# Kernel tuning notes

Hardware: AMD Instinct MI355X
Metric: run time of the kernel (lower is better)

The kernel has to match this reference:

```python
import jax, jax.numpy as jnp
import numpy as np

SCALE = 4          # cfg['stride']
S = 7              # rcnn_crop_size
MAX_SIDE = 64      # max proposal side length in voxels (matches setup_inputs)
# max feature-space crop length = MAX_SIDE/SCALE + 2 (floor/ceil expansion) = 18
WMAX = int(np.ceil((MAX_SIDE // SCALE + 2) / S)) + 1  # = 4, adaptive-pool window bound


def setup_inputs() -> dict:
    key = jax.random.key(0)
    k1, k2, k3, k4 = jax.random.split(key, 4)
    B, C = 2, 128
    D, H, W = 128, 256, 256
    f = jax.random.normal(k1, (B, C, D // SCALE, H // SCALE, W // SCALE), jnp.float32)
    inputs = jnp.zeros((B, 1, D, H, W), jnp.float32)  # only shape is used by forward
    N = 32
    b = jax.random.randint(k2, (N,), 0, B).astype(jnp.float32)
    score = jnp.ones((N,), jnp.float32)
    cz = jax.random.uniform(k3, (N,), minval=32.0, maxval=float(D - 32))
    cy = jax.random.uniform(jax.random.fold_in(k3, 1), (N,), minval=32.0, maxval=float(H - 32))
    cx = jax.random.uniform(jax.random.fold_in(k3, 2), (N,), minval=32.0, maxval=float(W - 32))
    sides = jax.random.randint(k4, (N, 3), 16, MAX_SIDE + 1).astype(jnp.float32)
    proposals = jnp.stack([b, score, cz, cy, cx, sides[:, 0], sides[:, 1], sides[:, 2]], axis=1)
    return {"f": f, "inputs": inputs, "proposals": proposals}


def _crop_pool(f, b, c0, L, feat_dims):
    """Adaptive max-pool3d of f[b, :, c0:c0+L] to [C,S,S,S] via fixed-size masked windows."""
    i = jnp.arange(S)
    # torch adaptive pooling: start=floor(i*L/S), end=ceil((i+1)*L/S)
    start = (i[:, None] * L[None, :]) // S                       # [S,3]
    end = ((i[:, None] + 1) * L[None, :] + S - 1) // S           # [S,3]
    idx = c0[None, :, None] + start[:, :, None] + jnp.arange(WMAX)[None, None, :]  # [S,3,WMAX]
    valid = idx < (c0[None, :, None] + end[:, :, None])
    idx = jnp.minimum(idx, jnp.asarray(feat_dims, jnp.int32)[None, :, None] - 1)
    iz, iy, ix = idx[:, 0], idx[:, 1], idx[:, 2]                 # each [S,WMAX]
    vz, vy, vx = valid[:, 0], valid[:, 1], valid[:, 2]
    # gather [C, S, WMAX, S, WMAX, S, WMAX]
    g = f[b][:, iz[:, :, None, None, None, None],
             iy[None, None, :, :, None, None],
             ix[None, None, None, None, :, :]]
    m = (vz[:, :, None, None, None, None]
         & vy[None, None, :, :, None, None]
         & vx[None, None, None, None, :, :])
    g = jnp.where(m[None], g, -jnp.inf)
    return g.max(axis=(2, 4, 6))  # [C, S, S, S]


def reference(f, inputs, proposals):
    D, H, W = inputs.shape[2:]
    feat_dims = (D // SCALE, H // SCALE, W // SCALE)
    b = proposals[:, 0].astype(jnp.int32)
    center = proposals[:, 2:5]
    side = proposals[:, 5:8]
    c0 = jnp.floor((center - side / 2) / SCALE).astype(jnp.int32)
    c1 = jnp.ceil((center + side / 2) / SCALE).astype(jnp.int32)
    lim = jnp.asarray(feat_dims, jnp.int32)
    c0 = jnp.maximum(c0, 0)
    c1 = jnp.minimum(c1, lim[None, :])
    L = c1 - c0  # [N,3] crop lengths per axis
    pooled = jax.vmap(lambda bb, cc, ll: _crop_pool(f, bb, cc, ll, feat_dims))(b, c0, L)
    return pooled  # [N, C, S, S, S]
```

## Files before the change

kernel.cpp:

```cpp
#include <hip/hip_runtime.h>
#include <math.h>


#define POOL_S 7
constexpr int C_CH = 128;
constexpr int FD = 32, FH = 64, FW = 64;
constexpr int OUT_PER_N = C_CH * POOL_S * POOL_S * POOL_S;
constexpr int TOTAL = 32 * OUT_PER_N;

__global__ __launch_bounds__(256) void crop_roi_kernel(
    const float* __restrict__ f,
    const float* __restrict__ proposals,
    float* __restrict__ out)
{
    int tid = blockIdx.x * blockDim.x + threadIdx.x;
    if (tid >= TOTAL) return;

    int ix = tid % 7;
    int iy = (tid / 7) % 7;
    int iz = (tid / 49) % 7;
    int c  = (tid / 343) % C_CH;
    int n  = tid / OUT_PER_N;

    const float* p = proposals + n * 8;
    int   b  = (int)p[0];
    float cz = p[2], cy = p[3], cx = p[4];
    float sz = p[5], sy = p[6], sx = p[7];

    int c0z = max((int)floorf((cz - sz * 0.5f) * 0.25f), 0);
    int c0y = max((int)floorf((cy - sy * 0.5f) * 0.25f), 0);
    int c0x = max((int)floorf((cx - sx * 0.5f) * 0.25f), 0);
    int c1z = min((int)ceilf((cz + sz * 0.5f) * 0.25f), FD);
    int c1y = min((int)ceilf((cy + sy * 0.5f) * 0.25f), FH);
    int c1x = min((int)ceilf((cx + sx * 0.5f) * 0.25f), FW);
    int Lz = c1z - c0z, Ly = c1y - c0y, Lx = c1x - c0x;

    int z0 = c0z + (iz * Lz) / 7, z1 = c0z + ((iz + 1) * Lz + 6) / 7;
    int y0 = c0y + (iy * Ly) / 7, y1 = c0y + ((iy + 1) * Ly + 6) / 7;
    int x0 = c0x + (ix * Lx) / 7, x1 = c0x + ((ix + 1) * Lx + 6) / 7;

    const float* fb = f + (size_t)(b * C_CH + c) * (FD * FH * FW);

    float m = -INFINITY;
    for (int z = z0; z < z1; ++z) {
        const float* fz = fb + z * (FH * FW);
        for (int y = y0; y < y1; ++y) {
            const float* fy = fz + y * FW;
            for (int x = x0; x < x1; ++x) {
                m = fmaxf(m, fy[x]);
            }
        }
    }
    out[tid] = m;
}

extern "C" void kernel_launch(void* const* d_in, const int* in_sizes, int n_in,
                              void* d_out, int out_size, void* d_ws, size_t ws_size,
                              hipStream_t stream) {
    const float* f         = (const float*)d_in[0];
    const float* proposals = (const float*)d_in[2];
    float* out             = (float*)d_out;

    const int block = 256;
    const int grid  = (TOTAL + block - 1) / block;
    crop_roi_kernel<<<grid, block, 0, stream>>>(f, proposals, out);
}
```

Before: 220.2 us.

## Stage each proposal's crop in LDS and pool windows from shared memory

Each block now handles one proposal and two channels. It first cooperatively loads a padded 17^3 crop of each channel into shared memory, clamping indices to the crop bounds, then computes the 7x7x7 adaptive max-pool windows from LDS. The x loop is replaced by four fixed loads with clamped indices, which relies on each window being at most 4 wide. This removes the redundant, poorly coalesced global reads caused by overlapping pooling windows. In exchange it always loads the full padded 17^3 volume even for small crops and adds a block-wide barrier.

```diff
diff --git a/kernel.cpp b/kernel.cpp
--- a/kernel.cpp
+++ b/kernel.cpp
@@ -2,56 +2,77 @@
 #include <math.h>
 
 
-#define POOL_S 7
 constexpr int C_CH = 128;
 constexpr int FD = 32, FH = 64, FW = 64;
-constexpr int OUT_PER_N = C_CH * POOL_S * POOL_S * POOL_S;
-constexpr int TOTAL = 32 * OUT_PER_N;
+constexpr int CH_VOL = FD * FH * FW;
+constexpr int LMAX = 17;
+constexpr int VOL = LMAX * LMAX * LMAX;
+constexpr int CPB = 2;
+constexpr int THREADS = 256;
 
-__global__ __launch_bounds__(256) void crop_roi_kernel(
+__global__ __launch_bounds__(THREADS) void crop_roi_kernel(
     const float* __restrict__ f,
     const float* __restrict__ proposals,
     float* __restrict__ out)
 {
-    int tid = blockIdx.x * blockDim.x + threadIdx.x;
-    if (tid >= TOTAL) return;
+    __shared__ float lds[CPB * VOL];
 
-    int ix = tid % 7;
-    int iy = (tid / 7) % 7;
-    int iz = (tid / 49) % 7;
-    int c  = (tid / 343) % C_CH;
-    int n  = tid / OUT_PER_N;
+    const int n    = blockIdx.x;
+    const int c0ch = blockIdx.y * CPB;
 
     const float* p = proposals + n * 8;
-    int   b  = (int)p[0];
-    float cz = p[2], cy = p[3], cx = p[4];
-    float sz = p[5], sy = p[6], sx = p[7];
+    const int   b  = (int)p[0];
+    const float cz = p[2], cy = p[3], cx = p[4];
+    const float sz = p[5], sy = p[6], sx = p[7];
 
-    int c0z = max((int)floorf((cz - sz * 0.5f) * 0.25f), 0);
-    int c0y = max((int)floorf((cy - sy * 0.5f) * 0.25f), 0);
-    int c0x = max((int)floorf((cx - sx * 0.5f) * 0.25f), 0);
-    int c1z = min((int)ceilf((cz + sz * 0.5f) * 0.25f), FD);
-    int c1y = min((int)ceilf((cy + sy * 0.5f) * 0.25f), FH);
-    int c1x = min((int)ceilf((cx + sx * 0.5f) * 0.25f), FW);
-    int Lz = c1z - c0z, Ly = c1y - c0y, Lx = c1x - c0x;
+    const int c0z = max((int)floorf((cz - sz * 0.5f) * 0.25f), 0);
+    const int c0y = max((int)floorf((cy - sy * 0.5f) * 0.25f), 0);
+    const int c0x = max((int)floorf((cx - sx * 0.5f) * 0.25f), 0);
+    const int c1z = min((int)ceilf((cz + sz * 0.5f) * 0.25f), FD);
+    const int c1y = min((int)ceilf((cy + sy * 0.5f) * 0.25f), FH);
+    const int c1x = min((int)ceilf((cx + sx * 0.5f) * 0.25f), FW);
+    const int Lz = c1z - c0z, Ly = c1y - c0y, Lx = c1x - c0x;
 
-    int z0 = c0z + (iz * Lz) / 7, z1 = c0z + ((iz + 1) * Lz + 6) / 7;
-    int y0 = c0y + (iy * Ly) / 7, y1 = c0y + ((iy + 1) * Ly + 6) / 7;
-    int x0 = c0x + (ix * Lx) / 7, x1 = c0x + ((ix + 1) * Lx + 6) / 7;
+    const float* fb = f + (size_t)(b * C_CH + c0ch) * CH_VOL
+                        + c0z * (FH * FW) + c0y * FW + c0x;
+    #pragma unroll 4
+    for (int e = threadIdx.x; e < CPB * VOL; e += THREADS) {
+        int cl = e / VOL;
+        int r  = e % VOL;
+        int z  = r / (LMAX * LMAX);
+        int y  = (r / LMAX) % LMAX;
+        int x  = r % LMAX;
+        int zc = min(z, Lz - 1);
+        int yc = min(y, Ly - 1);
+        int xc = min(x, Lx - 1);
+        lds[e] = fb[(size_t)cl * CH_VOL + zc * (FH * FW) + yc * FW + xc];
+    }
+    __syncthreads();
 
-    const float* fb = f + (size_t)(b * C_CH + c) * (FD * FH * FW);
+    for (int o = threadIdx.x; o < CPB * 343; o += THREADS) {
+        int cl = o / 343;
+        int r  = o % 343;
+        int iz = r / 49, iy = (r / 7) % 7, ix = r % 7;
 
-    float m = -INFINITY;
-    for (int z = z0; z < z1; ++z) {
-        const float* fz = fb + z * (FH * FW);
-        for (int y = y0; y < y1; ++y) {
-            const float* fy = fz + y * FW;
-            for (int x = x0; x < x1; ++x) {
-                m = fmaxf(m, fy[x]);
+        int zs = (iz * Lz) / 7, ze = ((iz + 1) * Lz + 6) / 7;
+        int ys = (iy * Ly) / 7, ye = ((iy + 1) * Ly + 6) / 7;
+        int xs = (ix * Lx) / 7, xe = ((ix + 1) * Lx + 6) / 7;
+
+        const float* Lp = lds + cl * VOL;
+        float m = -INFINITY;
+        for (int z = zs; z < ze; ++z) {
+            for (int y = ys; y < ye; ++y) {
+                int base = z * (LMAX * LMAX) + y * LMAX;
+                int xm = xe - 1;
+                float v0 = Lp[base + xs];
+                float v1 = Lp[base + min(xs + 1, xm)];
+                float v2 = Lp[base + min(xs + 2, xm)];
+                float v3 = Lp[base + min(xs + 3, xm)];
+                m = fmaxf(m, fmaxf(fmaxf(v0, v1), fmaxf(v2, v3)));
             }
         }
+        out[(size_t)(n * C_CH + c0ch) * 343 + o] = m;
     }
-    out[tid] = m;
 }
 
 extern "C" void kernel_launch(void* const* d_in, const int* in_sizes, int n_in,
@@ -61,7 +82,6 @@
     const float* proposals = (const float*)d_in[2];
     float* out             = (float*)d_out;
 
-    const int block = 256;
-    const int grid  = (TOTAL + block - 1) / block;
-    crop_roi_kernel<<<grid, block, 0, stream>>>(f, proposals, out);
+    dim3 grid(32, C_CH / CPB);
+    crop_roi_kernel<<<grid, THREADS, 0, stream>>>(f, proposals, out);
 }
```

After: 217.8 us. No clear change (-1.1%).
